# Kernel tuning notes

Hardware: AMD Instinct MI355X
Metric: run time of the kernel (lower is better)

The kernel has to match this reference:

```python
import jax, jax.numpy as jnp
import numpy as np

N_NODES = 50000
N_EDGES = 400000
N_GRAPHS = 256
F_IN = 128
HID = 64
HEADS = 4
N_CLS = 1


def setup_inputs() -> dict:
    key = jax.random.key(0)
    ks = jax.random.split(key, 16)
    inp = {
        "x": jax.random.normal(ks[0], (N_NODES, F_IN), dtype=jnp.float32),
        "edge_index": jax.random.randint(ks[1], (2, N_EDGES), 0, N_NODES, dtype=jnp.int32),
        "batch": jnp.sort(jax.random.randint(ks[2], (N_NODES,), 0, N_GRAPHS, dtype=jnp.int32)),
        # GCN layers
        "w1": jax.random.normal(ks[3], (F_IN, HID), dtype=jnp.float32) / np.sqrt(F_IN),
        "b1": jnp.zeros((HID,), jnp.float32),
        "w2": jax.random.normal(ks[4], (HID, HID), dtype=jnp.float32) / np.sqrt(HID),
        "b2": jnp.zeros((HID,), jnp.float32),
        "w3": jax.random.normal(ks[5], (HID, HID), dtype=jnp.float32) / np.sqrt(HID),
        "b3": jnp.zeros((HID,), jnp.float32),
        # GAT (heads=4, per-head dim HID, concat=False -> mean over heads)
        "gat_w": jax.random.normal(ks[6], (HID, HEADS * HID), dtype=jnp.float32) / np.sqrt(HID),
        "att_src": jax.random.normal(ks[7], (HEADS, HID), dtype=jnp.float32) / np.sqrt(HID),
        "att_dst": jax.random.normal(ks[8], (HEADS, HID), dtype=jnp.float32) / np.sqrt(HID),
        "gat_b": jnp.zeros((HID,), jnp.float32),
        # classifier 64 -> 32 -> 1
        "cw1": jax.random.normal(ks[9], (HID, HID // 2), dtype=jnp.float32) / np.sqrt(HID),
        "cb1": jnp.zeros((HID // 2,), jnp.float32),
        "cw2": jax.random.normal(ks[10], (HID // 2, N_CLS), dtype=jnp.float32) / np.sqrt(HID // 2),
        "cb2": jnp.zeros((N_CLS,), jnp.float32),
    }
    return inp


def _add_self_loops(edge_index, n):
    loops = jnp.arange(n, dtype=edge_index.dtype)
    src = jnp.concatenate([edge_index[0], loops])
    dst = jnp.concatenate([edge_index[1], loops])
    return src, dst


def _gcn(x, w, b, src, dst, norm, n):
    h = x @ w  # [N, out]
    msg = h[src] * norm[:, None]  # gather + per-edge scale
    out = jax.ops.segment_sum(msg, dst, num_segments=n)  # scatter-add
    return out + b


def _gat(x, w, att_src, att_dst, b, src, dst, n):
    h = (x @ w).reshape(n, HEADS, HID)  # [N,H,C]
    a_src = jnp.einsum("nhc,hc->nh", h, att_src)  # [N,H]
    a_dst = jnp.einsum("nhc,hc->nh", h, att_dst)
    e = jax.nn.leaky_relu(a_src[src] + a_dst[dst], negative_slope=0.2)  # [E,H]
    m = jax.ops.segment_max(e, dst, num_segments=n)  # stable segment softmax
    ex = jnp.exp(e - m[dst])
    denom = jax.ops.segment_sum(ex, dst, num_segments=n)
    alpha = ex / denom[dst]  # [E,H]
    out = jax.ops.segment_sum(alpha[:, :, None] * h[src], dst, num_segments=n)  # [N,H,C]
    return out.mean(axis=1) + b  # concat=False -> head mean


def reference(x, edge_index, batch, w1, b1, w2, b2, w3, b3,
              gat_w, att_src, att_dst, gat_b, cw1, cb1, cw2, cb2):
    n = x.shape[0]
    src, dst = _add_self_loops(edge_index, n)
    # symmetric GCN normalization deg^-1/2 (with self-loops), shared by all GCN layers
    deg = jax.ops.segment_sum(jnp.ones_like(dst, dtype=x.dtype), dst, num_segments=n)
    dinv = jnp.where(deg > 0, jax.lax.rsqrt(deg), 0.0)
    norm = dinv[src] * dinv[dst]  # [E']

    h = jax.nn.relu(_gcn(x, w1, b1, src, dst, norm, n))
    h = jax.nn.relu(_gcn(h, w2, b2, src, dst, norm, n))
    h = jax.nn.relu(_gcn(h, w3, b3, src, dst, norm, n))
    h = jax.nn.relu(_gat(h, gat_w, att_src, att_dst, gat_b, src, dst, n))

    # global mean pool per graph
    sums = jax.ops.segment_sum(h, batch, num_segments=N_GRAPHS)
    cnts = jax.ops.segment_sum(jnp.ones((n,), h.dtype), batch, num_segments=N_GRAPHS)
    pooled = sums / jnp.maximum(cnts, 1.0)[:, None]  # [G, HID]

    z = jax.nn.relu(pooled @ cw1 + cb1)
    return z @ cw2 + cb2  # [G, num_classes]
```

## Files before the change

kernel.cpp:

```cpp
#include <hip/hip_runtime.h>
#include <hip/hip_bf16.h>

#define N_NODES 50000
#define N_EDGES 400000
#define E_TOT   450000
#define N_GRAPHS 256
#define F_IN 128
#define HID 64
#define SCAN_NB 196

__global__ void k_deg(const int* __restrict__ dstp, int* __restrict__ degi) {
    int e = blockIdx.x * blockDim.x + threadIdx.x;
    if (e < N_EDGES) atomicAdd(&degi[dstp[e]], 1);
}

__global__ void k_dinv(const int* __restrict__ degi, float* __restrict__ dinv) {
    int i = blockIdx.x * blockDim.x + threadIdx.x;
    if (i < N_NODES) dinv[i] = rsqrtf(1.0f + (float)degi[i]);
}

__global__ void k_scan1(const int* __restrict__ degi, int* __restrict__ rowptr,
                        int* __restrict__ partial) {
    __shared__ int s[256];
    int i = blockIdx.x * 256 + threadIdx.x;
    int v = (i < N_NODES) ? (degi[i] + 1) : 0;
    s[threadIdx.x] = v;
    __syncthreads();
    for (int off = 1; off < 256; off <<= 1) {
        int t = (threadIdx.x >= off) ? s[threadIdx.x - off] : 0;
        __syncthreads();
        s[threadIdx.x] += t;
        __syncthreads();
    }
    if (i < N_NODES) rowptr[i] = s[threadIdx.x] - v;
    if (threadIdx.x == 255) partial[blockIdx.x] = s[255];
}

__global__ void k_scan2(int* __restrict__ partial) {
    __shared__ int s[256];
    int v = (threadIdx.x < SCAN_NB) ? partial[threadIdx.x] : 0;
    s[threadIdx.x] = v;
    __syncthreads();
    for (int off = 1; off < 256; off <<= 1) {
        int t = (threadIdx.x >= off) ? s[threadIdx.x - off] : 0;
        __syncthreads();
        s[threadIdx.x] += t;
        __syncthreads();
    }
    if (threadIdx.x < SCAN_NB) partial[threadIdx.x] = s[threadIdx.x] - v;
}

__global__ void k_scan3(int* __restrict__ rowptr, const int* __restrict__ partial) {
    int i = blockIdx.x * 256 + threadIdx.x;
    if (i < N_NODES) rowptr[i] += partial[blockIdx.x];
    if (i == 0) rowptr[N_NODES] = E_TOT;
}

__global__ void k_fill_self(const int* __restrict__ rowptr, const float* __restrict__ dinv,
                            int* __restrict__ csr_src, float* __restrict__ csr_norm,
                            int* __restrict__ cursor) {
    int i = blockIdx.x * blockDim.x + threadIdx.x;
    if (i >= N_NODES) return;
    int p = rowptr[i];
    csr_src[p] = i;
    float di = dinv[i];
    csr_norm[p] = di * di;
    cursor[i] = 1;
}

__global__ void k_fill_edge(const int* __restrict__ srcp, const int* __restrict__ dstp,
                            const int* __restrict__ rowptr, const float* __restrict__ dinv,
                            int* __restrict__ cursor, int* __restrict__ csr_src,
                            float* __restrict__ csr_norm) {
    int e = blockIdx.x * blockDim.x + threadIdx.x;
    if (e >= N_EDGES) return;
    int s = srcp[e], d = dstp[e];
    int p = rowptr[d] + atomicAdd(&cursor[d], 1);
    csr_src[p] = s;
    csr_norm[p] = dinv[s] * dinv[d];
}

#define FMA4(A, S, W)               \
    A.x = fmaf(S, W.x, A.x);        \
    A.y = fmaf(S, W.y, A.y);        \
    A.z = fmaf(S, W.z, A.z);        \
    A.w = fmaf(S, W.w, A.w);

template <int K, bool EPI>
__global__ __launch_bounds__(256) void k_gemm_v3(
        const float* __restrict__ x, const float* __restrict__ w,
        const float* __restrict__ bias, float* __restrict__ out, int nrows) {
    __shared__ float sw[64 * 64];
    const int tid = threadIdx.x;
    const int wave = tid >> 6, lane = tid & 63;
    const int g = lane >> 4, l16 = lane & 15;
    const int c0 = l16 * 4;
    const int r0 = blockIdx.x * 64 + wave * 16 + g * 4;
    constexpr int KV = K / 4;
    const int last = nrows - 1;
    const float4* __restrict__ x4 = (const float4*)x;
    const float4* __restrict__ p0 = x4 + (size_t)min(r0 + 0, last) * KV;
    const float4* __restrict__ p1 = x4 + (size_t)min(r0 + 1, last) * KV;
    const float4* __restrict__ p2 = x4 + (size_t)min(r0 + 2, last) * KV;
    const float4* __restrict__ p3 = x4 + (size_t)min(r0 + 3, last) * KV;
    float4 a0 = make_float4(0.f, 0.f, 0.f, 0.f);
    float4 a1 = a0, a2 = a0, a3 = a0;

    for (int kt = 0; kt < K / 64; ++kt) {
        __syncthreads();
        for (int i = tid; i < 64 * 64; i += 256) {
            int k = i >> 6, j = i & 63;
            sw[i] = w[(kt * 64 + k) * 64 + j];
        }
        __syncthreads();
        const int kb = kt * 16;
#pragma unroll 4
        for (int k4 = 0; k4 < 16; ++k4) {
            float4 xv0 = p0[kb + k4];
            float4 xv1 = p1[kb + k4];
            float4 xv2 = p2[kb + k4];
            float4 xv3 = p3[kb + k4];
            const float* swp = &sw[(k4 * 4) * 64 + c0];
            float4 wv0 = *(const float4*)(swp);
            float4 wv1 = *(const float4*)(swp + 64);
            float4 wv2 = *(const float4*)(swp + 128);
            float4 wv3 = *(const float4*)(swp + 192);
            FMA4(a0, xv0.x, wv0) FMA4(a1, xv1.x, wv0) FMA4(a2, xv2.x, wv0) FMA4(a3, xv3.x, wv0)
            FMA4(a0, xv0.y, wv1) FMA4(a1, xv1.y, wv1) FMA4(a2, xv2.y, wv1) FMA4(a3, xv3.y, wv1)
            FMA4(a0, xv0.z, wv2) FMA4(a1, xv1.z, wv2) FMA4(a2, xv2.z, wv2) FMA4(a3, xv3.z, wv2)
            FMA4(a0, xv0.w, wv3) FMA4(a1, xv1.w, wv3) FMA4(a2, xv2.w, wv3) FMA4(a3, xv3.w, wv3)
        }
    }
    float4 bv = make_float4(0.f, 0.f, 0.f, 0.f);
    if (EPI) bv = *(const float4*)(bias + c0);
    if (EPI) {
        a0.x = fmaxf(a0.x + bv.x, 0.f); a0.y = fmaxf(a0.y + bv.y, 0.f);
        a0.z = fmaxf(a0.z + bv.z, 0.f); a0.w = fmaxf(a0.w + bv.w, 0.f);
        a1.x = fmaxf(a1.x + bv.x, 0.f); a1.y = fmaxf(a1.y + bv.y, 0.f);
        a1.z = fmaxf(a1.z + bv.z, 0.f); a1.w = fmaxf(a1.w + bv.w, 0.f);
        a2.x = fmaxf(a2.x + bv.x, 0.f); a2.y = fmaxf(a2.y + bv.y, 0.f);
        a2.z = fmaxf(a2.z + bv.z, 0.f); a2.w = fmaxf(a2.w + bv.w, 0.f);
        a3.x = fmaxf(a3.x + bv.x, 0.f); a3.y = fmaxf(a3.y + bv.y, 0.f);
        a3.z = fmaxf(a3.z + bv.z, 0.f); a3.w = fmaxf(a3.w + bv.w, 0.f);
    }
    if (r0 + 0 < nrows) *(float4*)(out + (size_t)(r0 + 0) * 64 + c0) = a0;
    if (r0 + 1 < nrows) *(float4*)(out + (size_t)(r0 + 1) * 64 + c0) = a1;
    if (r0 + 2 < nrows) *(float4*)(out + (size_t)(r0 + 2) * 64 + c0) = a2;
    if (r0 + 3 < nrows) *(float4*)(out + (size_t)(r0 + 3) * 64 + c0) = a3;
}

__global__ void k_gcn_gather4(const int* __restrict__ rowptr, const int* __restrict__ csr_src,
                              const float* __restrict__ csr_norm, const float* __restrict__ t,
                              const float* __restrict__ b, float* __restrict__ out) {
    int node = (blockIdx.x * blockDim.x + threadIdx.x) >> 6;
    int lane = threadIdx.x & 63;
    if (node >= N_NODES) return;
    int sub = lane >> 4, l16 = lane & 15;
    int beg = rowptr[node], end = rowptr[node + 1];
    const float4* __restrict__ t4 = (const float4*)t;
    float4 acc = {0.f, 0.f, 0.f, 0.f};
    for (int p0 = beg; p0 < end; p0 += 4) {
        int p = p0 + sub;
        if (p < end) {
            int s = csr_src[p];
            float nm = csr_norm[p];
            float4 v = t4[(size_t)s * 16 + l16];
            acc.x = fmaf(nm, v.x, acc.x);
            acc.y = fmaf(nm, v.y, acc.y);
            acc.z = fmaf(nm, v.z, acc.z);
            acc.w = fmaf(nm, v.w, acc.w);
        }
    }
#pragma unroll
    for (int m = 16; m <= 32; m <<= 1) {
        acc.x += __shfl_xor(acc.x, m);
        acc.y += __shfl_xor(acc.y, m);
        acc.z += __shfl_xor(acc.z, m);
        acc.w += __shfl_xor(acc.w, m);
    }
    if (lane < 16) {
        float4 bv = ((const float4*)b)[l16];
        float4 r;
        r.x = fmaxf(acc.x + bv.x, 0.f);
        r.y = fmaxf(acc.y + bv.y, 0.f);
        r.z = fmaxf(acc.z + bv.z, 0.f);
        r.w = fmaxf(acc.w + bv.w, 0.f);
        ((float4*)out)[(size_t)node * 16 + l16] = r;
    }
}

__global__ void k_wat(const float* __restrict__ gat_w, const float* __restrict__ att_src,
                      const float* __restrict__ att_dst, float* __restrict__ wat) {
    int t = threadIdx.x;
    int q = t >> 6, cin = t & 63;
    int h = q >> 1;
    const float* av = (q & 1) ? att_dst : att_src;
    float acc = 0.f;
#pragma unroll
    for (int c = 0; c < 64; ++c)
        acc = fmaf(gat_w[cin * 256 + h * 64 + c], av[h * 64 + c], acc);
    wat[t] = acc;
}

__global__ void k_wbig(const float* __restrict__ gat_w, float* __restrict__ wbig) {
    int i = blockIdx.x * 256 + threadIdx.x;
    if (i >= 256 * 64) return;
    int k = i >> 6, c = i & 63;
    int h = k >> 6, cin = k & 63;
    wbig[i] = 0.25f * gat_w[cin * 256 + h * 64 + c];
}

__global__ void k_att2(const float* __restrict__ xin, const float* __restrict__ wat,
                       float* __restrict__ asrc, float* __restrict__ adst) {
    __shared__ float sw[512];
    for (int i = threadIdx.x; i < 512; i += 256) sw[i] = wat[i];
    __syncthreads();
    int node = (blockIdx.x * blockDim.x + threadIdx.x) >> 6;
    int lane = threadIdx.x & 63;
    if (node >= N_NODES) return;
    float val = xin[(size_t)node * 64 + lane];
#pragma unroll
    for (int q = 0; q < 8; ++q) {
        float p = val * sw[q * 64 + lane];
#pragma unroll
        for (int m = 1; m <= 32; m <<= 1) p += __shfl_xor(p, m);
        if (lane == q) {
            if (q & 1) adst[node * 4 + (q >> 1)] = p;
            else       asrc[node * 4 + (q >> 1)] = p;
        }
    }
}

static __device__ __forceinline__ float lrelu02(float v) {
    return v >= 0.f ? v : 0.2f * v;
}

__global__ void k_gat_alpha(const int* __restrict__ rowptr, const int* __restrict__ csr_src,
                            const float* __restrict__ asrc, const float* __restrict__ adst,
                            float* __restrict__ ebuf, float* __restrict__ denom) {
    int node = (blockIdx.x * blockDim.x + threadIdx.x) >> 6;
    int lane = threadIdx.x & 63;
    if (node >= N_NODES) return;
    int h = lane & 3, esub = lane >> 2;
    int beg = rowptr[node], end = rowptr[node + 1];
    float ad = adst[node * 4 + h];
    float m = -1e30f;
    for (int base = beg; base < end; base += 16) {
        int e = base + esub;
        if (e < end) {
            int s = csr_src[e];
            m = fmaxf(m, lrelu02(asrc[s * 4 + h] + ad));
        }
    }
#pragma unroll
    for (int mk = 4; mk <= 32; mk <<= 1) m = fmaxf(m, __shfl_xor(m, mk));
    float den = 0.f;
    for (int base = beg; base < end; base += 16) {
        int e = base + esub;
        if (e < end) {
            int s = csr_src[e];
            float ex = expf(lrelu02(asrc[s * 4 + h] + ad) - m);
            den += ex;
            ebuf[e * 4 + h] = ex;
        }
    }
#pragma unroll
    for (int mk = 4; mk <= 32; mk <<= 1) den += __shfl_xor(den, mk);
    if (lane < 4) denom[node * 4 + lane] = den;
}

__global__ void k_gat_wsum(const int* __restrict__ rowptr, const int* __restrict__ csr_src,
                           const float* __restrict__ ebuf, const float* __restrict__ denom,
                           const float* __restrict__ bufA, float* __restrict__ pcat) {
    int node = (blockIdx.x * blockDim.x + threadIdx.x) >> 6;
    int lane = threadIdx.x & 63;
    if (node >= N_NODES) return;
    int h = lane >> 4, l16 = lane & 15;
    int beg = rowptr[node], end = rowptr[node + 1];
    const float4* __restrict__ a4 = (const float4*)bufA;
    float4 acc = {0.f, 0.f, 0.f, 0.f};
    for (int p = beg; p < end; ++p) {
        int s = csr_src[p];
        float a = ebuf[p * 4 + h];
        float4 v = a4[(size_t)s * 16 + l16];
        acc.x = fmaf(a, v.x, acc.x);
        acc.y = fmaf(a, v.y, acc.y);
        acc.z = fmaf(a, v.z, acc.z);
        acc.w = fmaf(a, v.w, acc.w);
    }
    float inv = 1.0f / denom[node * 4 + h];
    acc.x *= inv; acc.y *= inv; acc.z *= inv; acc.w *= inv;
    ((float4*)pcat)[(size_t)node * 64 + lane] = acc;
}

__global__ void k_pool2(const int* __restrict__ batch, const float* __restrict__ h,
                        float* __restrict__ psum, float* __restrict__ pcnt) {
    int wave = (blockIdx.x * blockDim.x + threadIdx.x) >> 6;
    int lane = threadIdx.x & 63;
    int n0 = wave * 32;
    if (n0 >= N_NODES) return;
    int nend = min(n0 + 32, N_NODES);
    int cur = batch[n0];
    float acc = 0.f, cnt = 0.f;
    for (int n = n0; n < nend; ++n) {
        int g = batch[n];
        if (g != cur) {
            atomicAdd(&psum[cur * 64 + lane], acc);
            if (lane == 0) atomicAdd(&pcnt[cur], cnt);
            acc = 0.f; cnt = 0.f; cur = g;
        }
        acc += h[(size_t)n * 64 + lane];
        cnt += 1.f;
    }
    atomicAdd(&psum[cur * 64 + lane], acc);
    if (lane == 0) atomicAdd(&pcnt[cur], cnt);
}

__global__ void k_cls(const float* __restrict__ psum, const float* __restrict__ pcnt,
                      const float* __restrict__ cw1, const float* __restrict__ cb1,
                      const float* __restrict__ cw2, const float* __restrict__ cb2,
                      float* __restrict__ out) {
    int g = blockIdx.x;
    int j = threadIdx.x;
    __shared__ float sp[64];
    float rc = 1.0f / fmaxf(pcnt[g], 1.0f);
    sp[j] = psum[g * 64 + j] * rc;
    __syncthreads();
    float z = 0.f;
    if (j < 32) {
        float acc = 0.f;
#pragma unroll
        for (int k = 0; k < 64; ++k) acc = fmaf(sp[k], cw1[k * 32 + j], acc);
        acc += cb1[j];
        acc = fmaxf(acc, 0.f);
        z = acc * cw2[j];
    }
#pragma unroll
    for (int off = 32; off; off >>= 1) z += __shfl_down(z, off);
    if (j == 0) out[g] = z + cb2[0];
}

extern "C" void kernel_launch(void* const* d_in, const int* in_sizes, int n_in,
                              void* d_out, int out_size, void* d_ws, size_t ws_size,
                              hipStream_t stream) {
    const float* x       = (const float*)d_in[0];
    const int*   ei      = (const int*)d_in[1];
    const int*   batch   = (const int*)d_in[2];
    const float* w1      = (const float*)d_in[3];
    const float* b1      = (const float*)d_in[4];
    const float* w2      = (const float*)d_in[5];
    const float* b2      = (const float*)d_in[6];
    const float* w3      = (const float*)d_in[7];
    const float* b3      = (const float*)d_in[8];
    const float* gat_w   = (const float*)d_in[9];
    const float* att_src = (const float*)d_in[10];
    const float* att_dst = (const float*)d_in[11];
    const float* gat_b   = (const float*)d_in[12];
    const float* cw1     = (const float*)d_in[13];
    const float* cb1     = (const float*)d_in[14];
    const float* cw2     = (const float*)d_in[15];
    const float* cb2     = (const float*)d_in[16];
    float* out = (float*)d_out;

    const int* srcp = ei;
    const int* dstp = ei + N_EDGES;

    float* W = (float*)d_ws;
    size_t off = 0;
    float*    dinv    = W + off; off += N_NODES;
    int*      degi    = (int*)(W + off); off += N_NODES;
    int*      rowptr  = (int*)(W + off); off += N_NODES + 1;
    int*      partial = (int*)(W + off); off += 256;
    int*      cursor  = (int*)(W + off); off += N_NODES;
    int*      csr_src = (int*)(W + off); off += E_TOT;
    float*    csr_nrm = W + off; off += E_TOT;
    float*    bufT    = W + off; off += (size_t)N_NODES * HID;
    float*    bufA    = W + off; off += (size_t)N_NODES * HID;
    float*    bufB    = W + off; off += (size_t)N_NODES * HID;
    float*    pcat    = W + off; off += (size_t)N_NODES * 256;
    float*    asrc    = W + off; off += (size_t)N_NODES * 4;
    float*    adst    = W + off; off += (size_t)N_NODES * 4;
    float*    ebuf    = W + off; off += (size_t)E_TOT * 4;
    float*    denom   = W + off; off += (size_t)N_NODES * 4;
    float*    wat     = W + off; off += 512;
    float*    wbig    = W + off; off += 256 * 64;
    float*    psum    = W + off; off += (size_t)N_GRAPHS * HID;
    float*    pcnt    = W + off; off += N_GRAPHS;

    auto cdiv = [](int a, int b) { return (a + b - 1) / b; };

    hipMemsetAsync(degi, 0, N_NODES * sizeof(int), stream);
    hipMemsetAsync(psum, 0, (N_GRAPHS * HID + N_GRAPHS) * sizeof(float), stream);

    k_deg<<<cdiv(N_EDGES, 256), 256, 0, stream>>>(dstp, degi);
    k_dinv<<<cdiv(N_NODES, 256), 256, 0, stream>>>(degi, dinv);
    k_scan1<<<SCAN_NB, 256, 0, stream>>>(degi, rowptr, partial);
    k_scan2<<<1, 256, 0, stream>>>(partial);
    k_scan3<<<SCAN_NB, 256, 0, stream>>>(rowptr, partial);
    k_fill_self<<<cdiv(N_NODES, 256), 256, 0, stream>>>(rowptr, dinv, csr_src, csr_nrm, cursor);
    k_fill_edge<<<cdiv(N_EDGES, 256), 256, 0, stream>>>(srcp, dstp, rowptr, dinv, cursor,
                                                        csr_src, csr_nrm);

    const int nWV = cdiv(N_NODES * 64, 256);
    const int nGB = cdiv(N_NODES, 64);

    k_gemm_v3<F_IN, false><<<nGB, 256, 0, stream>>>(x, w1, nullptr, bufT, N_NODES);
    k_gcn_gather4<<<nWV, 256, 0, stream>>>(rowptr, csr_src, csr_nrm, bufT, b1, bufA);

    k_gemm_v3<HID, false><<<nGB, 256, 0, stream>>>(bufA, w2, nullptr, bufT, N_NODES);
    k_gcn_gather4<<<nWV, 256, 0, stream>>>(rowptr, csr_src, csr_nrm, bufT, b2, bufB);

    k_gemm_v3<HID, false><<<nGB, 256, 0, stream>>>(bufB, w3, nullptr, bufT, N_NODES);
    k_gcn_gather4<<<nWV, 256, 0, stream>>>(rowptr, csr_src, csr_nrm, bufT, b3, bufA);

    k_wat<<<1, 512, 0, stream>>>(gat_w, att_src, att_dst, wat);
    k_wbig<<<64, 256, 0, stream>>>(gat_w, wbig);
    k_att2<<<nWV, 256, 0, stream>>>(bufA, wat, asrc, adst);
    k_gat_alpha<<<nWV, 256, 0, stream>>>(rowptr, csr_src, asrc, adst, ebuf, denom);
    k_gat_wsum<<<nWV, 256, 0, stream>>>(rowptr, csr_src, ebuf, denom, bufA, pcat);
    k_gemm_v3<256, true><<<nGB, 256, 0, stream>>>(pcat, wbig, gat_b, bufB, N_NODES);

    k_pool2<<<cdiv(cdiv(N_NODES, 32) * 64, 256), 256, 0, stream>>>(batch, bufB, psum, pcnt);
    k_cls<<<N_GRAPHS, 64, 0, stream>>>(psum, pcnt, cw1, cb1, cw2, cb2, out);
}
```

Measured before the change: 459.8 us.

## Fuse setup kernels, merge memsets, and use persistent grid-stride gather kernels

Folds k_dinv into k_scan1 and k_fill_self into k_scan3, merges k_wat and k_wbig into one kernel, and combines the two memsets into one by placing degi next to psum. The GCN gather, GAT alpha and GAT weighted-sum kernels become grid-stride loops over a fixed 2048-block grid. The gather loops also software-prefetch the next edge's index and weight. The aim is fewer launches and less per-node wave launch cost, plus hidden index-load latency, at the cost of possible load imbalance across the fixed grid.

```diff
diff --git a/kernel.cpp b/kernel.cpp
--- a/kernel.cpp
+++ b/kernel.cpp
@@ -9,18 +9,23 @@
 #define HID 64
 #define SCAN_NB 196
 
+#define FMA4(A, S, W)               \
+    A.x = fmaf(S, W.x, A.x);        \
+    A.y = fmaf(S, W.y, A.y);        \
+    A.z = fmaf(S, W.z, A.z);        \
+    A.w = fmaf(S, W.w, A.w);
+
+static __device__ __forceinline__ float lrelu02(float v) {
+    return v >= 0.f ? v : 0.2f * v;
+}
+
 __global__ void k_deg(const int* __restrict__ dstp, int* __restrict__ degi) {
     int e = blockIdx.x * blockDim.x + threadIdx.x;
     if (e < N_EDGES) atomicAdd(&degi[dstp[e]], 1);
 }
 
-__global__ void k_dinv(const int* __restrict__ degi, float* __restrict__ dinv) {
-    int i = blockIdx.x * blockDim.x + threadIdx.x;
-    if (i < N_NODES) dinv[i] = rsqrtf(1.0f + (float)degi[i]);
-}
-
 __global__ void k_scan1(const int* __restrict__ degi, int* __restrict__ rowptr,
-                        int* __restrict__ partial) {
+                        int* __restrict__ partial, float* __restrict__ dinv) {
     __shared__ int s[256];
     int i = blockIdx.x * 256 + threadIdx.x;
     int v = (i < N_NODES) ? (degi[i] + 1) : 0;
@@ -32,7 +37,10 @@
         s[threadIdx.x] += t;
         __syncthreads();
     }
-    if (i < N_NODES) rowptr[i] = s[threadIdx.x] - v;
+    if (i < N_NODES) {
+        rowptr[i] = s[threadIdx.x] - v;
+        dinv[i] = rsqrtf((float)v);
+    }
     if (threadIdx.x == 255) partial[blockIdx.x] = s[255];
 }
 
@@ -50,22 +58,19 @@
     if (threadIdx.x < SCAN_NB) partial[threadIdx.x] = s[threadIdx.x] - v;
 }
 
-__global__ void k_scan3(int* __restrict__ rowptr, const int* __restrict__ partial) {
+__global__ void k_scan3(int* __restrict__ rowptr, const int* __restrict__ partial,
+                        const float* __restrict__ dinv, int* __restrict__ csr_src,
+                        float* __restrict__ csr_norm, int* __restrict__ cursor) {
     int i = blockIdx.x * 256 + threadIdx.x;
-    if (i < N_NODES) rowptr[i] += partial[blockIdx.x];
+    if (i < N_NODES) {
+        int rp = rowptr[i] + partial[blockIdx.x];
+        rowptr[i] = rp;
+        csr_src[rp] = i;
+        float di = dinv[i];
+        csr_norm[rp] = di * di;
+        cursor[i] = 1;
+    }
     if (i == 0) rowptr[N_NODES] = E_TOT;
-}
-
-__global__ void k_fill_self(const int* __restrict__ rowptr, const float* __restrict__ dinv,
-                            int* __restrict__ csr_src, float* __restrict__ csr_norm,
-                            int* __restrict__ cursor) {
-    int i = blockIdx.x * blockDim.x + threadIdx.x;
-    if (i >= N_NODES) return;
-    int p = rowptr[i];
-    csr_src[p] = i;
-    float di = dinv[i];
-    csr_norm[p] = di * di;
-    cursor[i] = 1;
 }
 
 __global__ void k_fill_edge(const int* __restrict__ srcp, const int* __restrict__ dstp,
@@ -79,12 +84,6 @@
     csr_src[p] = s;
     csr_norm[p] = dinv[s] * dinv[d];
 }
-
-#define FMA4(A, S, W)               \
-    A.x = fmaf(S, W.x, A.x);        \
-    A.y = fmaf(S, W.y, A.y);        \
-    A.z = fmaf(S, W.z, A.z);        \
-    A.w = fmaf(S, W.w, A.w);
 
 template <int K, bool EPI>
 __global__ __launch_bounds__(256) void k_gemm_v3(
@@ -149,48 +148,56 @@
     if (r0 + 3 < nrows) *(float4*)(out + (size_t)(r0 + 3) * 64 + c0) = a3;
 }
 
-__global__ void k_gcn_gather4(const int* __restrict__ rowptr, const int* __restrict__ csr_src,
-                              const float* __restrict__ csr_norm, const float* __restrict__ t,
-                              const float* __restrict__ b, float* __restrict__ out) {
-    int node = (blockIdx.x * blockDim.x + threadIdx.x) >> 6;
-    int lane = threadIdx.x & 63;
-    if (node >= N_NODES) return;
-    int sub = lane >> 4, l16 = lane & 15;
-    int beg = rowptr[node], end = rowptr[node + 1];
+__global__ __launch_bounds__(256) void k_gcn_gather_v3(
+        const int* __restrict__ rowptr, const int* __restrict__ csr_src,
+        const float* __restrict__ csr_norm, const float* __restrict__ t,
+        const float* __restrict__ b, float* __restrict__ out) {
+    const int gw = (blockIdx.x * 256 + threadIdx.x) >> 6;
+    const int nw = (gridDim.x * 256) >> 6;
+    const int lane = threadIdx.x & 63;
+    const int sub = lane >> 4, l16 = lane & 15;
     const float4* __restrict__ t4 = (const float4*)t;
-    float4 acc = {0.f, 0.f, 0.f, 0.f};
-    for (int p0 = beg; p0 < end; p0 += 4) {
-        int p = p0 + sub;
-        if (p < end) {
-            int s = csr_src[p];
-            float nm = csr_norm[p];
-            float4 v = t4[(size_t)s * 16 + l16];
-            acc.x = fmaf(nm, v.x, acc.x);
-            acc.y = fmaf(nm, v.y, acc.y);
-            acc.z = fmaf(nm, v.z, acc.z);
-            acc.w = fmaf(nm, v.w, acc.w);
-        }
-    }
-#pragma unroll
-    for (int m = 16; m <= 32; m <<= 1) {
-        acc.x += __shfl_xor(acc.x, m);
-        acc.y += __shfl_xor(acc.y, m);
-        acc.z += __shfl_xor(acc.z, m);
-        acc.w += __shfl_xor(acc.w, m);
-    }
-    if (lane < 16) {
-        float4 bv = ((const float4*)b)[l16];
-        float4 r;
-        r.x = fmaxf(acc.x + bv.x, 0.f);
-        r.y = fmaxf(acc.y + bv.y, 0.f);
-        r.z = fmaxf(acc.z + bv.z, 0.f);
-        r.w = fmaxf(acc.w + bv.w, 0.f);
-        ((float4*)out)[(size_t)node * 16 + l16] = r;
-    }
-}
-
-__global__ void k_wat(const float* __restrict__ gat_w, const float* __restrict__ att_src,
-                      const float* __restrict__ att_dst, float* __restrict__ wat) {
+    const float4 bv = ((const float4*)b)[l16];
+    for (int node = gw; node < N_NODES; node += nw) {
+        int beg = rowptr[node], end = rowptr[node + 1];
+        float4 acc = make_float4(0.f, 0.f, 0.f, 0.f);
+        int p = beg + sub;
+        bool vc = p < end;
+        int sc = 0; float nc = 0.f;
+        if (vc) { sc = csr_src[p]; nc = csr_norm[p]; }
+        while (vc) {
+            int pn = p + 4;
+            bool vn = pn < end;
+            int sn = 0; float nn = 0.f;
+            if (vn) { sn = csr_src[pn]; nn = csr_norm[pn]; }
+            float4 v = t4[(size_t)sc * 16 + l16];
+            acc.x = fmaf(nc, v.x, acc.x);
+            acc.y = fmaf(nc, v.y, acc.y);
+            acc.z = fmaf(nc, v.z, acc.z);
+            acc.w = fmaf(nc, v.w, acc.w);
+            p = pn; vc = vn; sc = sn; nc = nn;
+        }
+#pragma unroll
+        for (int m = 16; m <= 32; m <<= 1) {
+            acc.x += __shfl_xor(acc.x, m);
+            acc.y += __shfl_xor(acc.y, m);
+            acc.z += __shfl_xor(acc.z, m);
+            acc.w += __shfl_xor(acc.w, m);
+        }
+        if (lane < 16) {
+            float4 r;
+            r.x = fmaxf(acc.x + bv.x, 0.f);
+            r.y = fmaxf(acc.y + bv.y, 0.f);
+            r.z = fmaxf(acc.z + bv.z, 0.f);
+            r.w = fmaxf(acc.w + bv.w, 0.f);
+            ((float4*)out)[(size_t)node * 16 + l16] = r;
+        }
+    }
+}
+
+__global__ void k_wat2(const float* __restrict__ gat_w, const float* __restrict__ att_src,
+                       const float* __restrict__ att_dst, float* __restrict__ wat,
+                       float* __restrict__ wbig) {
     int t = threadIdx.x;
     int q = t >> 6, cin = t & 63;
     int h = q >> 1;
@@ -200,14 +207,11 @@
     for (int c = 0; c < 64; ++c)
         acc = fmaf(gat_w[cin * 256 + h * 64 + c], av[h * 64 + c], acc);
     wat[t] = acc;
-}
-
-__global__ void k_wbig(const float* __restrict__ gat_w, float* __restrict__ wbig) {
-    int i = blockIdx.x * 256 + threadIdx.x;
-    if (i >= 256 * 64) return;
-    int k = i >> 6, c = i & 63;
-    int h = k >> 6, cin = k & 63;
-    wbig[i] = 0.25f * gat_w[cin * 256 + h * 64 + c];
+    for (int i = t; i < 256 * 64; i += 512) {
+        int k = i >> 6, c = i & 63;
+        int hh = k >> 6, ci = k & 63;
+        wbig[i] = 0.25f * gat_w[ci * 256 + hh * 64 + c];
+    }
 }
 
 __global__ void k_att2(const float* __restrict__ xin, const float* __restrict__ wat,
@@ -231,66 +235,73 @@
     }
 }
 
-static __device__ __forceinline__ float lrelu02(float v) {
-    return v >= 0.f ? v : 0.2f * v;
-}
-
-__global__ void k_gat_alpha(const int* __restrict__ rowptr, const int* __restrict__ csr_src,
-                            const float* __restrict__ asrc, const float* __restrict__ adst,
-                            float* __restrict__ ebuf, float* __restrict__ denom) {
-    int node = (blockIdx.x * blockDim.x + threadIdx.x) >> 6;
-    int lane = threadIdx.x & 63;
-    if (node >= N_NODES) return;
-    int h = lane & 3, esub = lane >> 2;
-    int beg = rowptr[node], end = rowptr[node + 1];
-    float ad = adst[node * 4 + h];
-    float m = -1e30f;
-    for (int base = beg; base < end; base += 16) {
-        int e = base + esub;
-        if (e < end) {
-            int s = csr_src[e];
-            m = fmaxf(m, lrelu02(asrc[s * 4 + h] + ad));
-        }
-    }
-#pragma unroll
-    for (int mk = 4; mk <= 32; mk <<= 1) m = fmaxf(m, __shfl_xor(m, mk));
-    float den = 0.f;
-    for (int base = beg; base < end; base += 16) {
-        int e = base + esub;
-        if (e < end) {
-            int s = csr_src[e];
-            float ex = expf(lrelu02(asrc[s * 4 + h] + ad) - m);
-            den += ex;
-            ebuf[e * 4 + h] = ex;
-        }
-    }
-#pragma unroll
-    for (int mk = 4; mk <= 32; mk <<= 1) den += __shfl_xor(den, mk);
-    if (lane < 4) denom[node * 4 + lane] = den;
-}
-
-__global__ void k_gat_wsum(const int* __restrict__ rowptr, const int* __restrict__ csr_src,
-                           const float* __restrict__ ebuf, const float* __restrict__ denom,
-                           const float* __restrict__ bufA, float* __restrict__ pcat) {
-    int node = (blockIdx.x * blockDim.x + threadIdx.x) >> 6;
-    int lane = threadIdx.x & 63;
-    if (node >= N_NODES) return;
-    int h = lane >> 4, l16 = lane & 15;
-    int beg = rowptr[node], end = rowptr[node + 1];
+__global__ __launch_bounds__(256) void k_gat_alpha(
+        const int* __restrict__ rowptr, const int* __restrict__ csr_src,
+        const float* __restrict__ asrc, const float* __restrict__ adst,
+        float* __restrict__ ebuf, float* __restrict__ denom) {
+    const int gw = (blockIdx.x * 256 + threadIdx.x) >> 6;
+    const int nw = (gridDim.x * 256) >> 6;
+    const int lane = threadIdx.x & 63;
+    const int h = lane & 3, esub = lane >> 2;
+    for (int node = gw; node < N_NODES; node += nw) {
+        int beg = rowptr[node], end = rowptr[node + 1];
+        float ad = adst[node * 4 + h];
+        float m = -1e30f;
+        for (int base = beg; base < end; base += 16) {
+            int e = base + esub;
+            if (e < end) {
+                int s = csr_src[e];
+                m = fmaxf(m, lrelu02(asrc[s * 4 + h] + ad));
+            }
+        }
+#pragma unroll
+        for (int mk = 4; mk <= 32; mk <<= 1) m = fmaxf(m, __shfl_xor(m, mk));
+        float den = 0.f;
+        for (int base = beg; base < end; base += 16) {
+            int e = base + esub;
+            if (e < end) {
+                int s = csr_src[e];
+                float ex = expf(lrelu02(asrc[s * 4 + h] + ad) - m);
+                den += ex;
+                ebuf[e * 4 + h] = ex;
+            }
+        }
+#pragma unroll
+        for (int mk = 4; mk <= 32; mk <<= 1) den += __shfl_xor(den, mk);
+        if (lane < 4) denom[node * 4 + lane] = den;
+    }
+}
+
+__global__ __launch_bounds__(256) void k_gat_wsum(
+        const int* __restrict__ rowptr, const int* __restrict__ csr_src,
+        const float* __restrict__ ebuf, const float* __restrict__ denom,
+        const float* __restrict__ bufA, float* __restrict__ pcat) {
+    const int gw = (blockIdx.x * 256 + threadIdx.x) >> 6;
+    const int nw = (gridDim.x * 256) >> 6;
+    const int lane = threadIdx.x & 63;
+    const int h = lane >> 4, l16 = lane & 15;
     const float4* __restrict__ a4 = (const float4*)bufA;
-    float4 acc = {0.f, 0.f, 0.f, 0.f};
-    for (int p = beg; p < end; ++p) {
-        int s = csr_src[p];
-        float a = ebuf[p * 4 + h];
-        float4 v = a4[(size_t)s * 16 + l16];
-        acc.x = fmaf(a, v.x, acc.x);
-        acc.y = fmaf(a, v.y, acc.y);
-        acc.z = fmaf(a, v.z, acc.z);
-        acc.w = fmaf(a, v.w, acc.w);
-    }
-    float inv = 1.0f / denom[node * 4 + h];
-    acc.x *= inv; acc.y *= inv; acc.z *= inv; acc.w *= inv;
-    ((float4*)pcat)[(size_t)node * 64 + lane] = acc;
+    for (int node = gw; node < N_NODES; node += nw) {
+        int beg = rowptr[node], end = rowptr[node + 1];
+        float4 acc = make_float4(0.f, 0.f, 0.f, 0.f);
+        int p = beg;
+        int sc = csr_src[p];
+        float ac = ebuf[p * 4 + h];
+        while (p < end) {
+            int pn = p + 1;
+            int sn = 0; float an = 0.f;
+            if (pn < end) { sn = csr_src[pn]; an = ebuf[pn * 4 + h]; }
+            float4 v = a4[(size_t)sc * 16 + l16];
+            acc.x = fmaf(ac, v.x, acc.x);
+            acc.y = fmaf(ac, v.y, acc.y);
+            acc.z = fmaf(ac, v.z, acc.z);
+            acc.w = fmaf(ac, v.w, acc.w);
+            p = pn; sc = sn; ac = an;
+        }
+        float inv = 1.0f / denom[node * 4 + h];
+        acc.x *= inv; acc.y *= inv; acc.z *= inv; acc.w *= inv;
+        ((float4*)pcat)[(size_t)node * 64 + lane] = acc;
+    }
 }
 
 __global__ void k_pool2(const int* __restrict__ batch, const float* __restrict__ h,
@@ -368,8 +379,7 @@
     float* W = (float*)d_ws;
     size_t off = 0;
     float*    dinv    = W + off; off += N_NODES;
-    int*      degi    = (int*)(W + off); off += N_NODES;
-    int*      rowptr  = (int*)(W + off); off += N_NODES + 1;
+    int*      rowptr  = (int*)(W + off); off += N_NODES + 4;
     int*      partial = (int*)(W + off); off += 256;
     int*      cursor  = (int*)(W + off); off += N_NODES;
     int*      csr_src = (int*)(W + off); off += E_TOT;
@@ -384,40 +394,36 @@
     float*    denom   = W + off; off += (size_t)N_NODES * 4;
     float*    wat     = W + off; off += 512;
     float*    wbig    = W + off; off += 256 * 64;
+    int*      degi    = (int*)(W + off); off += N_NODES;
     float*    psum    = W + off; off += (size_t)N_GRAPHS * HID;
     float*    pcnt    = W + off; off += N_GRAPHS;
 
     auto cdiv = [](int a, int b) { return (a + b - 1) / b; };
 
-    hipMemsetAsync(degi, 0, N_NODES * sizeof(int), stream);
-    hipMemsetAsync(psum, 0, (N_GRAPHS * HID + N_GRAPHS) * sizeof(float), stream);
+    hipMemsetAsync(degi, 0, (N_NODES + N_GRAPHS * HID + N_GRAPHS) * sizeof(int), stream);
 
     k_deg<<<cdiv(N_EDGES, 256), 256, 0, stream>>>(dstp, degi);
-    k_dinv<<<cdiv(N_NODES, 256), 256, 0, stream>>>(degi, dinv);
-    k_scan1<<<SCAN_NB, 256, 0, stream>>>(degi, rowptr, partial);
+    k_scan1<<<SCAN_NB, 256, 0, stream>>>(degi, rowptr, partial, dinv);
     k_scan2<<<1, 256, 0, stream>>>(partial);
-    k_scan3<<<SCAN_NB, 256, 0, stream>>>(rowptr, partial);
-    k_fill_self<<<cdiv(N_NODES, 256), 256, 0, stream>>>(rowptr, dinv, csr_src, csr_nrm, cursor);
+    k_scan3<<<SCAN_NB, 256, 0, stream>>>(rowptr, partial, dinv, csr_src, csr_nrm, cursor);
     k_fill_edge<<<cdiv(N_EDGES, 256), 256, 0, stream>>>(srcp, dstp, rowptr, dinv, cursor,
                                                         csr_src, csr_nrm);
-
+    k_wat2<<<1, 512, 0, stream>>>(gat_w, att_src, att_dst, wat, wbig);
+
+    const int nGS = 2048;
     const int nWV = cdiv(N_NODES * 64, 256);
     const int nGB = cdiv(N_NODES, 64);
 
     k_gemm_v3<F_IN, false><<<nGB, 256, 0, stream>>>(x, w1, nullptr, bufT, N_NODES);
-    k_gcn_gather4<<<nWV, 256, 0, stream>>>(rowptr, csr_src, csr_nrm, bufT, b1, bufA);
-
+    k_gcn_gather_v3<<<nGS, 256, 0, stream>>>(rowptr, csr_src, csr_nrm, bufT, b1, bufA);
     k_gemm_v3<HID, false><<<nGB, 256, 0, stream>>>(bufA, w2, nullptr, bufT, N_NODES);
-    k_gcn_gather4<<<nWV, 256, 0, stream>>>(rowptr, csr_src, csr_nrm, bufT, b2, bufB);
-
+    k_gcn_gather_v3<<<nGS, 256, 0, stream>>>(rowptr, csr_src, csr_nrm, bufT, b2, bufB);
     k_gemm_v3<HID, false><<<nGB, 256, 0, stream>>>(bufB, w3, nullptr, bufT, N_NODES);
-    k_gcn_gather4<<<nWV, 256, 0, stream>>>(rowptr, csr_src, csr_nrm, bufT, b3, bufA);
-
-    k_wat<<<1, 512, 0, stream>>>(gat_w, att_src, att_dst, wat);
-    k_wbig<<<64, 256, 0, stream>>>(gat_w, wbig);
+    k_gcn_gather_v3<<<nGS, 256, 0, stream>>>(rowptr, csr_src, csr_nrm, bufT, b3, bufA);
+
     k_att2<<<nWV, 256, 0, stream>>>(bufA, wat, asrc, adst);
-    k_gat_alpha<<<nWV, 256, 0, stream>>>(rowptr, csr_src, asrc, adst, ebuf, denom);
-    k_gat_wsum<<<nWV, 256, 0, stream>>>(rowptr, csr_src, ebuf, denom, bufA, pcat);
+    k_gat_alpha<<<nGS, 256, 0, stream>>>(rowptr, csr_src, asrc, adst, ebuf, denom);
+    k_gat_wsum<<<nGS, 256, 0, stream>>>(rowptr, csr_src, ebuf, denom, bufA, pcat);
     k_gemm_v3<256, true><<<nGB, 256, 0, stream>>>(pcat, wbig, gat_b, bufB, N_NODES);
 
     k_pool2<<<cdiv(cdiv(N_NODES, 32) * 64, 256), 256, 0, stream>>>(batch, bufB, psum, pcnt);
```

Result: faster. 448.1 us (-2.6%).
